# Kernel tuning notes

Measured on AMD Instinct MI355X. Metric: run time of the kernel, lower is better.

## Reference

```python
import jax, jax.numpy as jnp
import numpy as np

HEADS = 16
DIM_HEAD = 64
SCALE = DIM_HEAD ** -0.5


def setup_inputs() -> dict:
    key = jax.random.key(0)
    k1, k2, k3, k4 = jax.random.split(key, 4)
    b, n, dim = 2, 2048, 1024
    inner = HEADS * DIM_HEAD  # 1024
    x = jax.random.normal(k1, (b, n, dim), dtype=jnp.float32)
    # binary keep-mask (multiplicative, as in the original module)
    seq_mask = (jax.random.uniform(k2, (b, n)) < 0.9).astype(jnp.float32)
    # weights stored [in, out] (transpose of torch Linear layout)
    w_qkv = jax.random.normal(k3, (dim, inner * 3), dtype=jnp.float32) * (dim ** -0.5)
    w_out = jax.random.normal(k4, (inner, dim), dtype=jnp.float32) * (inner ** -0.5)
    return {"x": x, "seq_mask": seq_mask, "w_qkv": w_qkv, "w_out": w_out}


def reference(x, seq_mask, w_qkv, w_out):
    b, n, dim = x.shape
    qkv = x @ w_qkv                                   # [b, n, 3*inner]
    q, k, v = jnp.split(qkv, 3, axis=-1)
    split_heads = lambda t: t.reshape(b, n, HEADS, DIM_HEAD).transpose(0, 2, 1, 3)
    q, k, v = split_heads(q), split_heads(k), split_heads(v)  # [b, h, n, d]
    dots = jnp.einsum('bhid,bhjd->bhij', q, k) * SCALE        # [b, h, n, n]
    # multiplicative mask, broadcast over heads and query index i; mask depends on key index j
    dots = dots * seq_mask[:, None, None, :]
    attn = jax.nn.softmax(dots, axis=-1)
    out = jnp.einsum('bhij,bhjd->bhid', attn, v)              # [b, h, n, d]
    out = out.transpose(0, 2, 1, 3).reshape(b, n, HEADS * DIM_HEAD)
    return out @ w_out                                        # dropout p=0 -> identity
```

## Files before the change

### kernel.cpp

```cpp
#include <hip/hip_runtime.h>
#include <hip/hip_bf16.h>

using bf16 = __hip_bfloat16;
typedef __attribute__((ext_vector_type(8))) short short8;
typedef __attribute__((ext_vector_type(4))) float floatx4;
typedef __attribute__((ext_vector_type(16))) float floatx16;

#define MFMA_BF16(a, b, c) __builtin_amdgcn_mfma_f32_16x16x32_bf16((a), (b), (c), 0, 0, 0)
#define MFMA32(a, b, c) __builtin_amdgcn_mfma_f32_32x32x16_bf16((a), (b), (c), 0, 0, 0)

__device__ __forceinline__ void gload_lds16(const bf16* g, bf16* l) {
  __builtin_amdgcn_global_load_lds((__attribute__((address_space(1))) void*)g,
                                   (__attribute__((address_space(3))) void*)l,
                                   16, 0, 0);
}

__device__ __forceinline__ unsigned short bfbits(float f) {
  bf16 b = __float2bfloat16(f);
  return *reinterpret_cast<unsigned short*>(&b);
}

__device__ __forceinline__ int swz32(int r) { return (r & 7) ^ ((r >> 3) & 3); }

#define KSCALE 0.18033688011112042f

__global__ __launch_bounds__(256)
void probemask_k(const void* __restrict__ msrc, bf16* __restrict__ dst,
                 int* __restrict__ flag) {
  __shared__ int any;
  const int tid = threadIdx.x;
  if (tid == 0) any = 0;
  __syncthreads();
  const unsigned* mw = (const unsigned*)msrc;
  int bad = 0;
#pragma unroll
  for (int i = 0; i < 4; i++) {
    unsigned w = mw[tid * 4 + i];
    if (w != 0u && w != 0x3F800000u) bad = 1;
  }
  if (bad) atomicOr(&any, 1);
  __syncthreads();
  const int isbf = any;
  if (tid == 0) flag[0] = isbf;
  if (isbf) {
#pragma unroll
    for (int i = 0; i < 2; i++)
      ((int4*)dst)[tid * 2 + i] = ((const int4*)msrc)[tid * 2 + i];
  } else {
#pragma unroll
    for (int i = 0; i < 4; i++) {
      float4 v = ((const float4*)msrc)[tid * 4 + i];
      int o = tid * 16 + i * 4;
      dst[o + 0] = __float2bfloat16(v.x);
      dst[o + 1] = __float2bfloat16(v.y);
      dst[o + 2] = __float2bfloat16(v.z);
      dst[o + 3] = __float2bfloat16(v.w);
    }
  }
}

__global__ __launch_bounds__(256)
void cvt_k(const void* __restrict__ src, bf16* __restrict__ dst, int n,
           const int* __restrict__ flag) {
  if (*flag) return;
  int i = (blockIdx.x * 256 + threadIdx.x) * 4;
  if (i >= n) return;
  float4 v = ((const float4*)src)[i >> 2];
  dst[i + 0] = __float2bfloat16(v.x);
  dst[i + 1] = __float2bfloat16(v.y);
  dst[i + 2] = __float2bfloat16(v.z);
  dst[i + 3] = __float2bfloat16(v.w);
}

__global__ __launch_bounds__(256)
void transpose2_k(const void* __restrict__ in0, bf16* __restrict__ out0,
                  const void* __restrict__ in1, bf16* __restrict__ out1,
                  const int* __restrict__ flag) {
  __shared__ bf16 tile[32][33];
  const int isbf = *flag;
  constexpr int R = 1024;
  const void* in;
  bf16* out;
  int C, bx;
  if (blockIdx.x < 96) { in = in0; out = out0; C = 3072; bx = blockIdx.x * 32; }
  else                 { in = in1; out = out1; C = 1024; bx = (blockIdx.x - 96) * 32; }
  int by = blockIdx.y * 32;
  int tx = threadIdx.x & 31, ty = threadIdx.x >> 5;
#pragma unroll
  for (int i = 0; i < 4; i++) {
    size_t idx = (size_t)(by + ty + i * 8) * C + bx + tx;
    tile[ty + i * 8][tx] =
        isbf ? ((const bf16*)in)[idx] : __float2bfloat16(((const float*)in)[idx]);
  }
  __syncthreads();
#pragma unroll
  for (int i = 0; i < 4; i++)
    out[(size_t)(bx + ty + i * 8) * R + by + tx] = tile[tx][ty + i * 8];
}

template <int MODE>
__global__ __launch_bounds__(256, 2)
void gemm_k(const bf16* __restrict__ A, const bf16* __restrict__ Aalt,
            const bf16* __restrict__ Bt,
            bf16* __restrict__ Qo, bf16* __restrict__ Ko, bf16* __restrict__ Vo,
            void* __restrict__ Co, const bf16* __restrict__ Mk,
            const int* __restrict__ flag) {
  constexpr int K = 1024;
  __shared__ __align__(16) bf16 As[128 * 32];
  __shared__ __align__(16) bf16 Bs[128 * 32];

  const int tid = threadIdx.x;
  const int lane = tid & 63;
  const int wv = tid >> 6;
  const int wm = wv & 1, wn = wv >> 1;
  const int l15 = lane & 15, quad = lane >> 4;

  const int bm = blockIdx.y * 128;
  const int bn = blockIdx.x * 128;

  const int sml = tid >> 2;
  const int sg = (tid & 3) ^ ((sml >> 1) & 3);

  const int isbf = *flag;
  const bf16* Ab = (MODE == 0 && isbf) ? Aalt : A;

  floatx4 acc[4][4] = {};

  for (int k0 = 0; k0 < K; k0 += 32) {
    __syncthreads();
    const bf16* a0 = Ab + (size_t)(bm + sml) * K + k0 + sg * 8;
    gload_lds16(a0, &As[tid * 8]);
    gload_lds16(a0 + (size_t)64 * K, &As[2048 + tid * 8]);
    const bf16* b0 = Bt + (size_t)(bn + sml) * K + k0 + sg * 8;
    gload_lds16(b0, &Bs[tid * 8]);
    gload_lds16(b0 + (size_t)64 * K, &Bs[2048 + tid * 8]);
    __syncthreads();

    short8 af[4], bfr[4];
#pragma unroll
    for (int mi = 0; mi < 4; mi++) {
      int m = wm * 64 + mi * 16 + l15;
      af[mi] = *(const short8*)&As[m * 32 + ((quad ^ ((m >> 1) & 3)) * 8)];
    }
#pragma unroll
    for (int ni = 0; ni < 4; ni++) {
      int n = wn * 64 + ni * 16 + l15;
      bfr[ni] = *(const short8*)&Bs[n * 32 + ((quad ^ ((n >> 1) & 3)) * 8)];
    }
#pragma unroll
    for (int mi = 0; mi < 4; mi++)
#pragma unroll
      for (int ni = 0; ni < 4; ni++)
        acc[mi][ni] = MFMA_BF16(af[mi], bfr[ni], acc[mi][ni]);
  }

#pragma unroll
  for (int mi = 0; mi < 4; mi++) {
    const int row0 = bm + wm * 64 + mi * 16 + quad * 4;
#pragma unroll
    for (int ni = 0; ni < 4; ni++) {
      const int col = bn + wn * 64 + ni * 16 + l15;
      if (MODE == 0) {
        const int sec = col >> 10;
        const int cc = col & 1023;
        const int h = cc >> 6, d = cc & 63;
        const int b_idx = row0 >> 11;
        const int nn0 = row0 & 2047;
        if (sec == 0) {
          bf16* dst = Qo + (size_t)(b_idx * 16 + h) * 131072 + (size_t)nn0 * 64 + d;
#pragma unroll
          for (int r = 0; r < 4; r++) dst[r * 64] = __float2bfloat16(acc[mi][ni][r]);
        } else if (sec == 1) {
          const bf16* mrow = Mk + (size_t)b_idx * 2048 + nn0;
          bf16* dst = Ko + (size_t)(b_idx * 16 + h) * 131072 + (size_t)nn0 * 64 + d;
#pragma unroll
          for (int r = 0; r < 4; r++)
            dst[r * 64] = __float2bfloat16(acc[mi][ni][r] * KSCALE *
                                           __bfloat162float(mrow[r]));
        } else {
          bf16* dst = Vo + (size_t)(b_idx * 16 + h) * 131072 + (size_t)d * 2048 + nn0;
#pragma unroll
          for (int r = 0; r < 4; r++) dst[r] = __float2bfloat16(acc[mi][ni][r]);
        }
      } else {
        if (isbf) {
          bf16* C2 = (bf16*)Co;
#pragma unroll
          for (int r = 0; r < 4; r++)
            C2[(size_t)(row0 + r) * 1024 + col] = __float2bfloat16(acc[mi][ni][r]);
        } else {
          float* C2 = (float*)Co;
#pragma unroll
          for (int r = 0; r < 4; r++)
            C2[(size_t)(row0 + r) * 1024 + col] = acc[mi][ni][r];
        }
      }
    }
  }
}

__global__ __launch_bounds__(256, 2)
void flash_k(const bf16* __restrict__ Q, const bf16* __restrict__ K,
             const bf16* __restrict__ VT, bf16* __restrict__ AO) {
  __shared__ __align__(16) bf16 Ks[2][4096];
  __shared__ __align__(16) bf16 Vs[2][4096];
  __shared__ __align__(16) bf16 Ps[8192];

  const int tid = threadIdx.x;
  const int lane = tid & 63;
  const int w = tid >> 6;
  const int l31 = lane & 31;
  const int l5h = lane >> 5;
  const int sw = swz32(l31);

  const int qt = blockIdx.x & 15;
  const int hl = blockIdx.x >> 4;
  const int b_idx = hl >> 4, h = hl & 15;

  const bf16* Qh = Q + (size_t)hl * 131072;
  const bf16* Kh = K + (size_t)hl * 131072;
  const bf16* Vh = VT + (size_t)hl * 131072;

  const int qbase = qt * 128 + w * 32;
  const int qrow = qbase + l31;

  short8 qf[4];
#pragma unroll
  for (int c = 0; c < 4; c++)
    qf[c] = *(const short8*)&Qh[(size_t)qrow * 64 + c * 16 + l5h * 8];

  floatx16 o_acc[2] = {};
  float rsum = 0.f;

  bf16* Psw = Ps + w * 2048;

  const int sjj = tid >> 3;
  const int sgp = (tid & 7) ^ swz32(sjj);

  gload_lds16(&Kh[(size_t)sjj * 64 + sgp * 8], &Ks[0][tid * 8]);
  gload_lds16(&Kh[(size_t)(32 + sjj) * 64 + sgp * 8], &Ks[0][2048 + tid * 8]);
  gload_lds16(&Vh[(size_t)sjj * 2048 + sgp * 8], &Vs[0][tid * 8]);
  gload_lds16(&Vh[(size_t)(32 + sjj) * 2048 + sgp * 8], &Vs[0][2048 + tid * 8]);

  for (int it = 0; it < 32; ++it) {
    const int b = it & 1;
    __syncthreads();
    if (it < 31) {
      const int j1 = (it + 1) * 64;
      gload_lds16(&Kh[(size_t)(j1 + sjj) * 64 + sgp * 8], &Ks[b ^ 1][tid * 8]);
      gload_lds16(&Kh[(size_t)(j1 + 32 + sjj) * 64 + sgp * 8], &Ks[b ^ 1][2048 + tid * 8]);
      gload_lds16(&Vh[(size_t)sjj * 2048 + j1 + sgp * 8], &Vs[b ^ 1][tid * 8]);
      gload_lds16(&Vh[(size_t)(32 + sjj) * 2048 + j1 + sgp * 8], &Vs[b ^ 1][2048 + tid * 8]);
    }

    floatx16 s[2] = {};
#pragma unroll
    for (int kt = 0; kt < 2; kt++) {
      const int key = kt * 32 + l31;
#pragma unroll
      for (int c = 0; c < 4; c++) {
        const int g = c * 2 + l5h;
        short8 kf = *(const short8*)&Ks[b][key * 64 + ((g ^ sw) * 8)];
        s[kt] = MFMA32(kf, qf[c], s[kt]);
      }
    }

    float rs = 0.f;
#pragma unroll
    for (int kt = 0; kt < 2; kt++)
#pragma unroll
      for (int r = 0; r < 16; r++) {
        const float p = __builtin_amdgcn_exp2f(s[kt][r]);
        s[kt][r] = p;
        rs += p;
      }
    rs += __shfl_xor(rs, 32, 64);
    rsum += rs;

#pragma unroll
    for (int kt = 0; kt < 2; kt++)
#pragma unroll
      for (int rg = 0; rg < 4; rg++) {
        ushort4 u;
        u.x = bfbits(s[kt][rg * 4 + 0]);
        u.y = bfbits(s[kt][rg * 4 + 1]);
        u.z = bfbits(s[kt][rg * 4 + 2]);
        u.w = bfbits(s[kt][rg * 4 + 3]);
        const int g = kt * 4 + rg;
        *(ushort4*)&Psw[l31 * 64 + ((g ^ sw) * 8) + l5h * 4] = u;
      }
    __builtin_amdgcn_wave_barrier();

    short8 pf[4];
#pragma unroll
    for (int c = 0; c < 4; c++) {
      const int g = c * 2 + l5h;
      pf[c] = *(const short8*)&Psw[l31 * 64 + ((g ^ sw) * 8)];
    }

#pragma unroll
    for (int dt = 0; dt < 2; dt++) {
      const int d = dt * 32 + l31;
#pragma unroll
      for (int c = 0; c < 4; c++) {
        const int g = c * 2 + l5h;
        short8 vf = *(const short8*)&Vs[b][d * 64 + ((g ^ sw) * 8)];
        o_acc[dt] = MFMA32(vf, pf[c], o_acc[dt]);
      }
    }
  }

  const float rinv = 1.f / rsum;
  bf16* orow = AO + (size_t)(b_idx * 2048 + qbase + l31) * 1024 + h * 64;
#pragma unroll
  for (int dt = 0; dt < 2; dt++)
#pragma unroll
    for (int rg = 0; rg < 4; rg++) {
      ushort4 u;
      u.x = bfbits(o_acc[dt][rg * 4 + 0] * rinv);
      u.y = bfbits(o_acc[dt][rg * 4 + 1] * rinv);
      u.z = bfbits(o_acc[dt][rg * 4 + 2] * rinv);
      u.w = bfbits(o_acc[dt][rg * 4 + 3] * rinv);
      *(ushort4*)&orow[dt * 32 + rg * 8 + l5h * 4] = u;
    }
}

extern "C" void kernel_launch(void* const* d_in, const int* in_sizes, int n_in,
                              void* d_out, int out_size, void* d_ws, size_t ws_size,
                              hipStream_t stream) {
  const void* x     = d_in[0];
  const void* mask  = d_in[1];
  const void* w_qkv = d_in[2];
  const void* w_out = d_in[3];

  bf16* ws    = (bf16*)d_ws;
  bf16* xb    = ws;
  bf16* AO    = ws;
  bf16* wqkvT = ws + 4194304;
  bf16* woutT = wqkvT + 3145728;
  bf16* Qb    = woutT + 1048576;
  bf16* Kb    = Qb + 4194304;
  bf16* maskb = Kb + 4194304;
  int*  flag  = (int*)(maskb + 4096);
  bf16* VT    = (bf16*)d_out;

  probemask_k<<<1, 256, 0, stream>>>(mask, maskb, flag);
  cvt_k<<<4096, 256, 0, stream>>>(x, xb, 4194304, flag);
  transpose2_k<<<dim3(128, 32), 256, 0, stream>>>(w_qkv, wqkvT, w_out, woutT, flag);
  gemm_k<0><<<dim3(24, 32), 256, 0, stream>>>(xb, (const bf16*)x, wqkvT, Qb, Kb, VT,
                                              nullptr, maskb, flag);
  flash_k<<<512, 256, 0, stream>>>(Qb, Kb, VT, AO);
  gemm_k<1><<<dim3(8, 32), 256, 0, stream>>>(AO, nullptr, woutT, nullptr, nullptr,
                                             nullptr, d_out, nullptr, flag);
}
```

Before: 193.4 us.

## Replace LDS round-trip for P fragments with permlane32 swaps in flash kernel

When the compiler has the permlane32_swap builtin, the attention kernel now rebuilds the bf16 P operand for the PV MFMA through cross-half-wave register swaps instead of writing to and reading back from a shared-memory P buffer. This removes the 16 KB Ps array and its LDS traffic and wave barrier. Launch bounds are raised from 2 to 4 blocks per SIMD/CU, which relies on the lower LDS use and may force register limits and spills. The fallback path keeps the old LDS method.

```diff
diff --git a/kernel.cpp b/kernel.cpp
--- a/kernel.cpp
+++ b/kernel.cpp
@@ -5,9 +5,16 @@
 typedef __attribute__((ext_vector_type(8))) short short8;
 typedef __attribute__((ext_vector_type(4))) float floatx4;
 typedef __attribute__((ext_vector_type(16))) float floatx16;
+typedef __attribute__((ext_vector_type(4))) int int4v;
 
 #define MFMA_BF16(a, b, c) __builtin_amdgcn_mfma_f32_16x16x32_bf16((a), (b), (c), 0, 0, 0)
 #define MFMA32(a, b, c) __builtin_amdgcn_mfma_f32_32x32x16_bf16((a), (b), (c), 0, 0, 0)
+
+#if defined(__has_builtin)
+#if __has_builtin(__builtin_amdgcn_permlane32_swap)
+#define HAS_PLSWAP 1
+#endif
+#endif
 
 __device__ __forceinline__ void gload_lds16(const bf16* g, bf16* l) {
   __builtin_amdgcn_global_load_lds((__attribute__((address_space(1))) void*)g,
@@ -18,6 +25,10 @@
 __device__ __forceinline__ unsigned short bfbits(float f) {
   bf16 b = __float2bfloat16(f);
   return *reinterpret_cast<unsigned short*>(&b);
+}
+
+__device__ __forceinline__ unsigned pk2(float a, float b) {
+  return (unsigned)bfbits(a) | ((unsigned)bfbits(b) << 16);
 }
 
 __device__ __forceinline__ int swz32(int r) { return (r & 7) ^ ((r >> 3) & 3); }
@@ -199,12 +210,14 @@
   }
 }
 
-__global__ __launch_bounds__(256, 2)
+__global__ __launch_bounds__(256, 4)
 void flash_k(const bf16* __restrict__ Q, const bf16* __restrict__ K,
              const bf16* __restrict__ VT, bf16* __restrict__ AO) {
   __shared__ __align__(16) bf16 Ks[2][4096];
   __shared__ __align__(16) bf16 Vs[2][4096];
+#ifndef HAS_PLSWAP
   __shared__ __align__(16) bf16 Ps[8192];
+#endif
 
   const int tid = threadIdx.x;
   const int lane = tid & 63;
@@ -232,7 +245,9 @@
   floatx16 o_acc[2] = {};
   float rsum = 0.f;
 
+#ifndef HAS_PLSWAP
   bf16* Psw = Ps + w * 2048;
+#endif
 
   const int sjj = tid >> 3;
   const int sgp = (tid & 7) ^ swz32(sjj);
@@ -277,6 +292,31 @@
     rs += __shfl_xor(rs, 32, 64);
     rsum += rs;
 
+    short8 pf[4];
+#ifdef HAS_PLSWAP
+#pragma unroll
+    for (int kt = 0; kt < 2; kt++) {
+      unsigned pd[4][2];
+#pragma unroll
+      for (int rg = 0; rg < 4; rg++) {
+        pd[rg][0] = pk2(s[kt][rg * 4 + 0], s[kt][rg * 4 + 1]);
+        pd[rg][1] = pk2(s[kt][rg * 4 + 2], s[kt][rg * 4 + 3]);
+      }
+#pragma unroll
+      for (int cp = 0; cp < 2; cp++) {
+        auto ra = __builtin_amdgcn_permlane32_swap(pd[cp * 2][0], pd[cp * 2 + 1][0],
+                                                   false, false);
+        auto rb = __builtin_amdgcn_permlane32_swap(pd[cp * 2][1], pd[cp * 2 + 1][1],
+                                                   false, false);
+        int4v pi;
+        pi[0] = (int)ra[0];
+        pi[1] = (int)rb[0];
+        pi[2] = (int)ra[1];
+        pi[3] = (int)rb[1];
+        pf[kt * 2 + cp] = *(short8*)&pi;
+      }
+    }
+#else
 #pragma unroll
     for (int kt = 0; kt < 2; kt++)
 #pragma unroll
@@ -290,13 +330,12 @@
         *(ushort4*)&Psw[l31 * 64 + ((g ^ sw) * 8) + l5h * 4] = u;
       }
     __builtin_amdgcn_wave_barrier();
-
-    short8 pf[4];
 #pragma unroll
     for (int c = 0; c < 4; c++) {
       const int g = c * 2 + l5h;
       pf[c] = *(const short8*)&Psw[l31 * 64 + ((g ^ sw) * 8)];
     }
+#endif
 
 #pragma unroll
     for (int dt = 0; dt < 2; dt++) {
```

After: 203.9 us. 5.4% more time.
